# Kernel tuning notes

Measured on AMD Instinct MI355X. Metric: run time of the kernel, lower is better.

## Reference

```python
import jax, jax.numpy as jnp
import numpy as np

EPS = 1e-5
GROUPS = 32
K = 7  # correlation kernel size (min(7, 14))


def group_norm(x, w, b):
    B, C, H, W = x.shape
    xg = x.reshape(B, GROUPS, C // GROUPS, H, W)
    m = xg.mean(axis=(2, 3, 4), keepdims=True)
    v = xg.var(axis=(2, 3, 4), keepdims=True)
    xg = (xg - m) * jax.lax.rsqrt(v + EPS)
    return xg.reshape(B, C, H, W) * w[None, :, None, None] + b[None, :, None, None]


def conv1x1(x, w):  # w: [O, C]
    return jnp.einsum('bchw,oc->bohw', x, w)


def setup_inputs() -> dict:
    key = jax.random.key(0)
    ks = jax.random.split(key, 16)
    C, CC = 256, 64
    d = {}
    d['template_feat'] = jax.random.normal(ks[0], (32, C, 14, 14), jnp.float32)
    d['search_feat'] = jax.random.normal(ks[1], (32, C, 64, 64), jnp.float32)
    s1 = 1.0 / np.sqrt(C)
    d['w_t'] = jax.random.normal(ks[2], (CC, C), jnp.float32) * s1
    d['gn_t_w'] = jnp.ones((CC,), jnp.float32)
    d['gn_t_b'] = jnp.zeros((CC,), jnp.float32)
    d['w_s'] = jax.random.normal(ks[3], (CC, C), jnp.float32) * s1
    d['gn_s_w'] = jnp.ones((CC,), jnp.float32)
    d['gn_s_b'] = jnp.zeros((CC,), jnp.float32)
    d['w_p1'] = jax.random.normal(ks[4], (CC, CC, 3, 3), jnp.float32) * (1.0 / np.sqrt(CC * 9))
    d['gn_p_w'] = jnp.ones((CC,), jnp.float32)
    d['gn_p_b'] = jnp.zeros((CC,), jnp.float32)
    d['w_p2'] = jax.random.normal(ks[5], (1, CC), jnp.float32) * (1.0 / np.sqrt(CC))
    d['b_p2'] = jnp.zeros((1,), jnp.float32)
    return d


def reference(template_feat, search_feat, w_t, gn_t_w, gn_t_b, w_s, gn_s_w, gn_s_b,
              w_p1, gn_p_w, gn_p_b, w_p2, b_p2):
    B, _, Hs, Ws = search_feat.shape
    CC = w_t.shape[0]

    t = jax.nn.relu(group_norm(conv1x1(template_feat, w_t), gn_t_w, gn_t_b))   # [B,CC,14,14]
    s = jax.nn.relu(group_norm(conv1x1(search_feat, w_s), gn_s_w, gn_s_b))     # [B,CC,Hs,Ws]

    # global correlation: adaptive pool template to (1,1) == mean
    t_global = t.mean(axis=(2, 3), keepdims=True)
    global_corr = s * t_global

    # local depthwise correlation: adaptive pool 14x14 -> 7x7 (exact 2x2 mean)
    Ht = t.shape[2]
    r = Ht // K
    t_kernel = t.reshape(B, CC, K, r, K, r).mean(axis=(3, 5))                  # [B,CC,7,7]

    # batched per-sample depthwise conv: fold batch into groups
    x = s.reshape(1, B * CC, Hs, Ws)
    kern = t_kernel.reshape(B * CC, 1, K, K)
    local = jax.lax.conv_general_dilated(
        x, kern, window_strides=(1, 1), padding=[(K // 2, K // 2)] * 2,
        dimension_numbers=('NCHW', 'OIHW', 'NCHW'),
        feature_group_count=B * CC)
    local_corr = local.reshape(B, CC, Hs, Ws)

    corr = global_corr + local_corr

    # post_corr: 3x3 conv -> GN -> ReLU -> 1x1 conv (+bias)
    y = jax.lax.conv_general_dilated(
        corr, w_p1, window_strides=(1, 1), padding='SAME',
        dimension_numbers=('NCHW', 'OIHW', 'NCHW'))
    y = jax.nn.relu(group_norm(y, gn_p_w, gn_p_b))
    out = conv1x1(y, w_p2) + b_p2[None, :, None, None]                          # [B,1,Hs,Ws]
    return out
```

## Files before the change

### kernel.cpp

```cpp
#include <hip/hip_runtime.h>

#define EPS 1e-5f


typedef __attribute__((ext_vector_type(8))) short short8;
typedef __attribute__((ext_vector_type(4))) float floatx4;

__device__ __forceinline__ unsigned short f2bf(float x) {
    union { float f; unsigned u; } v; v.f = x;
    unsigned r = v.u + 0x7FFFu + ((v.u >> 16) & 1u);
    return (unsigned short)(r >> 16);
}
__device__ __forceinline__ float bf2f(unsigned short h) {
    union { unsigned u; float f; } v; v.u = ((unsigned)h) << 16;
    return v.f;
}

__global__ __launch_bounds__(256) void k1_template(
    const float* __restrict__ tmpl, const float* __restrict__ w_t,
    const float* __restrict__ gnw, const float* __restrict__ gnb,
    float* __restrict__ t_global, float* __restrict__ t_kernel)
{
    int b = blockIdx.x >> 1, h = blockIdx.x & 1;
    int tid = threadIdx.x;
    __shared__ float T[32][197];
    __shared__ float sums[32], sumsq[32], A[32], Bb[32];
    int p = tid;
    if (p < 196) {
        float acc[32];
        #pragma unroll
        for (int o = 0; o < 32; ++o) acc[o] = 0.f;
        const float* xb = tmpl + b * 256 * 196 + p;
        const float* wb = w_t + (h * 32) * 256;
        for (int c = 0; c < 256; ++c) {
            float xv = xb[c * 196];
            #pragma unroll
            for (int o = 0; o < 32; ++o) acc[o] += xv * wb[o * 256 + c];
        }
        #pragma unroll
        for (int o = 0; o < 32; ++o) T[o][p] = acc[o];
    }
    __syncthreads();
    if (tid < 32) {
        float s = 0.f, s2 = 0.f;
        for (int q = 0; q < 196; ++q) { float v = T[tid][q]; s += v; s2 += v * v; }
        sums[tid] = s; sumsq[tid] = s2;
    }
    __syncthreads();
    if (tid < 16) {
        float S  = sums[2 * tid] + sums[2 * tid + 1];
        float S2 = sumsq[2 * tid] + sumsq[2 * tid + 1];
        float mean = S * (1.f / 392.f);
        float var  = S2 * (1.f / 392.f) - mean * mean;
        float inv  = rsqrtf(var + EPS);
        for (int e = 0; e < 2; ++e) {
            int c = 2 * tid + e, gc = h * 32 + c;
            float a = gnw[gc] * inv;
            A[c] = a; Bb[c] = gnb[gc] - mean * a;
        }
    }
    __syncthreads();
    if (p < 196) {
        #pragma unroll
        for (int o = 0; o < 32; ++o) {
            float v = A[o] * T[o][p] + Bb[o];
            T[o][p] = v > 0.f ? v : 0.f;
        }
    }
    __syncthreads();
    if (tid < 32) {
        int c = tid, gc = h * 32 + c;
        float s = 0.f;
        for (int q = 0; q < 196; ++q) s += T[c][q];
        t_global[b * 64 + gc] = s * (1.f / 196.f);
        for (int t = 0; t < 49; ++t) {
            int ky = t / 7, kx = t - 7 * ky;
            float v = T[c][(2 * ky) * 14 + 2 * kx]     + T[c][(2 * ky) * 14 + 2 * kx + 1]
                    + T[c][(2 * ky + 1) * 14 + 2 * kx] + T[c][(2 * ky + 1) * 14 + 2 * kx + 1];
            t_kernel[(b * 64 + gc) * 49 + t] = v * 0.25f;
        }
    }
}

__global__ __launch_bounds__(256) void k2_gemm_s(
    const float* __restrict__ x, const float* __restrict__ w,
    float* __restrict__ sraw)
{
    int b = blockIdx.y;
    int p0 = blockIdx.x << 8;
    int tid = threadIdx.x;
    int tx = tid & 31, ty = tid >> 5;
    __shared__ float Xs[16][256];
    __shared__ float Ws[16][68];
    float acc[8][8];
    #pragma unroll
    for (int j = 0; j < 8; ++j)
        #pragma unroll
        for (int k = 0; k < 8; ++k) acc[j][k] = 0.f;
    const float* xb = x + ((long)b << 20) + p0;
    for (int c0 = 0; c0 < 256; c0 += 16) {
        __syncthreads();
        #pragma unroll
        for (int l = 0; l < 16; ++l)
            Xs[l][tid] = xb[(c0 + l) * 4096 + tid];
        #pragma unroll
        for (int l = 0; l < 4; ++l) {
            int flat = tid + (l << 8);
            int o = flat >> 4, cc = flat & 15;
            Ws[cc][o] = w[o * 256 + c0 + cc];
        }
        __syncthreads();
        #pragma unroll
        for (int cc = 0; cc < 16; ++cc) {
            float xv[8], wv[8];
            #pragma unroll
            for (int k = 0; k < 8; ++k) xv[k] = Xs[cc][tx + (k << 5)];
            #pragma unroll
            for (int j = 0; j < 8; ++j) wv[j] = Ws[cc][(ty << 3) + j];
            #pragma unroll
            for (int j = 0; j < 8; ++j)
                #pragma unroll
                for (int k = 0; k < 8; ++k) acc[j][k] += wv[j] * xv[k];
        }
    }
    float* ob = sraw + ((long)b << 18) + p0;
    #pragma unroll
    for (int j = 0; j < 8; ++j) {
        int o = (ty << 3) + j;
        #pragma unroll
        for (int k = 0; k < 8; ++k)
            ob[(o << 12) + tx + (k << 5)] = acc[j][k];
    }
}

__global__ __launch_bounds__(256) void k_stats(
    const float* __restrict__ src, const float* __restrict__ gnw, const float* __restrict__ gnb,
    float* __restrict__ A, float* __restrict__ Bc)
{
    int g = blockIdx.x, b = blockIdx.y;
    int tid = threadIdx.x;
    const float* base = src + (((long)b * 64 + 2 * g) << 12);
    float s = 0.f, s2 = 0.f;
    for (int l = 0; l < 32; ++l) {
        float v = base[tid + (l << 8)];
        s += v; s2 += v * v;
    }
    #pragma unroll
    for (int off = 32; off > 0; off >>= 1) {
        s  += __shfl_down(s, off, 64);
        s2 += __shfl_down(s2, off, 64);
    }
    __shared__ float rs[4], rs2[4];
    int wid = tid >> 6, lane = tid & 63;
    if (lane == 0) { rs[wid] = s; rs2[wid] = s2; }
    __syncthreads();
    if (tid == 0) {
        float S = rs[0] + rs[1] + rs[2] + rs[3];
        float S2 = rs2[0] + rs2[1] + rs2[2] + rs2[3];
        float mean = S * (1.f / 8192.f);
        float var  = S2 * (1.f / 8192.f) - mean * mean;
        float inv  = rsqrtf(var + EPS);
        for (int e = 0; e < 2; ++e) {
            int c = 2 * g + e;
            float a = gnw[c] * inv;
            A[b * 64 + c] = a;
            Bc[b * 64 + c] = gnb[c] - mean * a;
        }
    }
}

__global__ __launch_bounds__(256) void k4_corr(
    const float* __restrict__ sraw, const float* __restrict__ A, const float* __restrict__ Bc,
    const float* __restrict__ t_global, const float* __restrict__ t_kernel,
    float* __restrict__ corr)
{
    int bc = blockIdx.x;
    int tid = threadIdx.x;
    __shared__ float tile[70 * 70];
    __shared__ float ker[49];
    float a = A[bc], bb = Bc[bc], tg = t_global[bc];
    for (int i = tid; i < 4900; i += 256) tile[i] = 0.f;
    if (tid < 49) ker[tid] = t_kernel[bc * 49 + tid];
    __syncthreads();
    const float* sb = sraw + ((long)bc << 12);
    for (int i = tid; i < 4096; i += 256) {
        int y = i >> 6, xx = i & 63;
        float v = a * sb[i] + bb;
        tile[(y + 3) * 70 + xx + 3] = v > 0.f ? v : 0.f;
    }
    __syncthreads();
    int x = tid & 63, ys = (tid >> 6) << 4;
    float acc[16];
    #pragma unroll
    for (int j = 0; j < 16; ++j) acc[j] = 0.f;
    #pragma unroll
    for (int kx = 0; kx < 7; ++kx) {
        float col[22];
        #pragma unroll
        for (int j = 0; j < 22; ++j) col[j] = tile[(ys + j) * 70 + x + kx];
        #pragma unroll
        for (int ky = 0; ky < 7; ++ky) {
            float kv = ker[ky * 7 + kx];
            #pragma unroll
            for (int j = 0; j < 16; ++j) acc[j] += kv * col[j + ky];
        }
    }
    float* ob = corr + ((long)bc << 12);
    #pragma unroll
    for (int j = 0; j < 16; ++j) {
        float sval = tile[(ys + j + 3) * 70 + x + 3];
        ob[((ys + j) << 6) + x] = acc[j] + sval * tg;
    }
}

__global__ __launch_bounds__(256) void k_t(
    const float* __restrict__ corr, unsigned short* __restrict__ corrT)
{
    int py = blockIdx.x, b = blockIdx.y;
    int tid = threadIdx.x;
    __shared__ float T[64][65];
    {
        int c0 = tid >> 6, px = tid & 63;
        const float* src = corr + (((long)b * 64) << 12) + (py << 6) + px;
        #pragma unroll
        for (int i = 0; i < 16; ++i) {
            int c = c0 + (i << 2);
            T[c][px] = src[(long)c << 12];
        }
    }
    __syncthreads();
    int ob = tid & 7, pxw = tid >> 3;
    unsigned short* dst = corrT + ((((b << 12)) + (py << 6)) << 6);
    #pragma unroll
    for (int i = 0; i < 2; ++i) {
        int p = pxw + (i << 5);
        unsigned w0 = (unsigned)f2bf(T[8 * ob + 0][p]) | ((unsigned)f2bf(T[8 * ob + 1][p]) << 16);
        unsigned w1 = (unsigned)f2bf(T[8 * ob + 2][p]) | ((unsigned)f2bf(T[8 * ob + 3][p]) << 16);
        unsigned w2 = (unsigned)f2bf(T[8 * ob + 4][p]) | ((unsigned)f2bf(T[8 * ob + 5][p]) << 16);
        unsigned w3 = (unsigned)f2bf(T[8 * ob + 6][p]) | ((unsigned)f2bf(T[8 * ob + 7][p]) << 16);
        uint4 val = {w0, w1, w2, w3};
        *(uint4*)(dst + ((long)p << 6) + (ob << 3)) = val;
    }
}

__global__ __launch_bounds__(256) void k_w(
    const float* __restrict__ w1, unsigned short* __restrict__ wpk)
{
    int i = blockIdx.x * 256 + threadIdx.x;
    if (i >= 36864) return;
    int c = i >> 11;
    int rem = i & 2047;
    int oc = rem >> 5;
    int k = rem & 31;
    int tap = c >> 1;
    int ic = ((c & 1) << 5) + k;
    wpk[i] = f2bf(w1[oc * 576 + ic * 9 + tap]);
}

__global__ __launch_bounds__(256) void k5_mfma(
    const unsigned short* __restrict__ corrT, const unsigned short* __restrict__ wpk,
    unsigned short* __restrict__ y)
{
    int b = blockIdx.y, py0 = blockIdx.x << 2;
    int tid = threadIdx.x;
    int wave = tid >> 6, lane = tid & 63, q = lane >> 4, l15 = lane & 15;
    __shared__ short tile[25344];

    for (int u = tid; u < 3168; u += 256) {
        int icblk = u & 7, rc = u >> 3;
        int row = rc / 66, col = rc - 66 * row;
        int py = py0 - 1 + row, px = col - 1;
        short8 v = {0, 0, 0, 0, 0, 0, 0, 0};
        if (py >= 0 && py < 64 && px >= 0 && px < 64)
            v = *(const short8*)(corrT + (((b << 12) + (py << 6) + px) << 6) + (icblk << 3));
        int sw = icblk ^ (col & 7);
        *(short8*)&tile[(rc << 6) + (sw << 3)] = v;
    }
    __syncthreads();

    floatx4 acc[4][4];
    #pragma unroll
    for (int i = 0; i < 4; ++i)
        #pragma unroll
        for (int ot = 0; ot < 4; ++ot) acc[i][ot] = (floatx4){0.f, 0.f, 0.f, 0.f};

    int pt0 = wave << 2;
    int rowb[4], colb[4];
    #pragma unroll
    for (int i = 0; i < 4; ++i) {
        int p = ((pt0 + i) << 4) + l15;
        rowb[i] = p >> 6;
        colb[i] = p & 63;
    }
    #pragma unroll
    for (int c = 0; c < 18; ++c) {
        const int tap = c >> 1, ky = tap / 3, kx = tap % 3, h = c & 1;
        short8 bfr[4], afr[4];
        #pragma unroll
        for (int ot = 0; ot < 4; ++ot)
            bfr[ot] = *(const short8*)(wpk + ((c << 6) + (ot << 4) + l15) * 32 + (q << 3));
        #pragma unroll
        for (int i = 0; i < 4; ++i) {
            int row = rowb[i] + ky, col = colb[i] + kx;
            int sw = ((h << 2) + q) ^ (col & 7);
            afr[i] = *(const short8*)&tile[((row * 66 + col) << 6) + (sw << 3)];
        }
        #pragma unroll
        for (int i = 0; i < 4; ++i)
            #pragma unroll
            for (int ot = 0; ot < 4; ++ot)
                acc[i][ot] = __builtin_amdgcn_mfma_f32_16x16x32_bf16(afr[i], bfr[ot], acc[i][ot], 0, 0, 0);
    }
    #pragma unroll
    for (int i = 0; i < 4; ++i) {
        #pragma unroll
        for (int r = 0; r < 4; ++r) {
            int p = ((pt0 + i) << 4) + (q << 2) + r;
            int py = py0 + (p >> 6), pxc = p & 63;
            int base = ((b << 12) + (py << 6) + pxc) << 6;
            #pragma unroll
            for (int ot = 0; ot < 4; ++ot)
                y[base + (ot << 4) + l15] = f2bf(acc[i][ot][r]);
        }
    }
}

__global__ __launch_bounds__(256) void k_sy1(
    const unsigned short* __restrict__ y, float* __restrict__ P1, float* __restrict__ P2)
{
    int sl = blockIdx.x, b = blockIdx.y;
    int tid = threadIdx.x;
    int ocp = tid & 31, px0 = tid >> 5;
    const unsigned* yp = (const unsigned*)y;
    float se = 0, s2e = 0, so = 0, s2o = 0;
    for (int k = 0; k < 64; ++k) {
        int px = (sl << 9) + (k << 3) + px0;
        unsigned u = yp[(((b << 12) + px) << 5) + ocp];
        float f0 = bf2f((unsigned short)(u & 0xFFFF));
        float f1 = bf2f((unsigned short)(u >> 16));
        se += f0; s2e += f0 * f0; so += f1; s2o += f1 * f1;
    }
    se += __shfl_down(se, 32, 64);  s2e += __shfl_down(s2e, 32, 64);
    so += __shfl_down(so, 32, 64);  s2o += __shfl_down(s2o, 32, 64);
    __shared__ float R[4][32][4];
    int w = tid >> 6, l = tid & 63;
    if (l < 32) { R[w][l][0] = se; R[w][l][1] = s2e; R[w][l][2] = so; R[w][l][3] = s2o; }
    __syncthreads();
    if (tid < 32) {
        float a0 = 0, a1 = 0, a2 = 0, a3 = 0;
        for (int w2 = 0; w2 < 4; ++w2) {
            a0 += R[w2][tid][0]; a1 += R[w2][tid][1]; a2 += R[w2][tid][2]; a3 += R[w2][tid][3];
        }
        int idx = ((b << 3) + sl) << 6;
        P1[idx + 2 * tid]     = a0; P2[idx + 2 * tid]     = a1;
        P1[idx + 2 * tid + 1] = a2; P2[idx + 2 * tid + 1] = a3;
    }
}

__global__ __launch_bounds__(64) void k_sy2(
    const float* __restrict__ P1, const float* __restrict__ P2,
    const float* __restrict__ gnw, const float* __restrict__ gnb,
    float* __restrict__ A, float* __restrict__ Bc)
{
    int b = blockIdx.x, c = threadIdx.x;
    float s = 0, s2 = 0;
    for (int sl = 0; sl < 8; ++sl) {
        int idx = (((b << 3) + sl) << 6) + c;
        s += P1[idx]; s2 += P2[idx];
    }
    float sp = __shfl_xor(s, 1, 64), s2p = __shfl_xor(s2, 1, 64);
    float S = s + sp, S2 = s2 + s2p;
    float mean = S * (1.f / 8192.f);
    float var  = S2 * (1.f / 8192.f) - mean * mean;
    float inv  = rsqrtf(var + EPS);
    float a = gnw[c] * inv;
    A[b * 64 + c] = a;
    Bc[b * 64 + c] = gnb[c] - mean * a;
}

__global__ __launch_bounds__(256) void k6_nhwc(
    const unsigned short* __restrict__ y, const float* __restrict__ A, const float* __restrict__ Bc,
    const float* __restrict__ w2, const float* __restrict__ b2, float* __restrict__ out)
{
    int b = blockIdx.y;
    int px0 = blockIdx.x << 9;
    int tid = threadIdx.x, wave = tid >> 6, lane = tid & 63;
    int ocp = lane & 31, ph = lane >> 5;
    int c0 = 2 * ocp;
    float a0 = A[b * 64 + c0],     b0 = Bc[b * 64 + c0],     w20 = w2[c0];
    float a1 = A[b * 64 + c0 + 1], b1 = Bc[b * 64 + c0 + 1], w21 = w2[c0 + 1];
    float bias = b2[0];
    const unsigned* yp = (const unsigned*)y;
    for (int i = 0; i < 64; ++i) {
        int px = px0 + (i << 3) + (wave << 1) + ph;
        unsigned u = yp[(((b << 12) + px) << 5) + ocp];
        float f0 = bf2f((unsigned short)(u & 0xFFFF));
        float f1 = bf2f((unsigned short)(u >> 16));
        float v0 = a0 * f0 + b0; v0 = v0 > 0.f ? v0 : 0.f;
        float v1 = a1 * f1 + b1; v1 = v1 > 0.f ? v1 : 0.f;
        float val = w20 * v0 + w21 * v1;
        #pragma unroll
        for (int m = 16; m >= 1; m >>= 1) val += __shfl_xor(val, m, 64);
        if (ocp == 0) out[(b << 12) + px] = val + bias;
    }
}

extern "C" void kernel_launch(void* const* d_in, const int* in_sizes, int n_in,
                              void* d_out, int out_size, void* d_ws, size_t ws_size,
                              hipStream_t stream)
{
    const float* tmpl   = (const float*)d_in[0];
    const float* search = (const float*)d_in[1];
    const float* w_t    = (const float*)d_in[2];
    const float* gn_t_w = (const float*)d_in[3];
    const float* gn_t_b = (const float*)d_in[4];
    const float* w_s    = (const float*)d_in[5];
    const float* gn_s_w = (const float*)d_in[6];
    const float* gn_s_b = (const float*)d_in[7];
    const float* w_p1   = (const float*)d_in[8];
    const float* gn_p_w = (const float*)d_in[9];
    const float* gn_p_b = (const float*)d_in[10];
    const float* w_p2   = (const float*)d_in[11];
    const float* b_p2   = (const float*)d_in[12];
    float* out = (float*)d_out;
    float* ws  = (float*)d_ws;

    float* TG   = ws;
    float* TK   = ws + 2048;
    float* AS   = ws + 102400;
    float* BS   = ws + 104448;
    float* AY   = ws + 106496;
    float* BY   = ws + 108544;
    float* P1   = ws + 110592;
    float* P2   = ws + 126976;
    unsigned short* WPK = (unsigned short*)(ws + 143360);
    float* SRAW = ws + 163840;
    float* CORR = ws + 163840 + 8388608;
    unsigned short* YRAW  = (unsigned short*)SRAW;
    unsigned short* CORRT = (unsigned short*)(SRAW + 4194304);

    k1_template<<<64, 256, 0, stream>>>(tmpl, w_t, gn_t_w, gn_t_b, TG, TK);
    k_w<<<144, 256, 0, stream>>>(w_p1, WPK);
    k2_gemm_s<<<dim3(16, 32), 256, 0, stream>>>(search, w_s, SRAW);
    k_stats<<<dim3(32, 32), 256, 0, stream>>>(SRAW, gn_s_w, gn_s_b, AS, BS);
    k4_corr<<<2048, 256, 0, stream>>>(SRAW, AS, BS, TG, TK, CORR);
    k_t<<<dim3(64, 32), 256, 0, stream>>>(CORR, CORRT);
    k5_mfma<<<dim3(16, 32), 256, 0, stream>>>(CORRT, WPK, YRAW);
    k_sy1<<<dim3(8, 32), 256, 0, stream>>>(YRAW, P1, P2);
    k_sy2<<<32, 64, 0, stream>>>(P1, P2, gn_p_w, gn_p_b, AY, BY);
    k6_nhwc<<<dim3(8, 32), 256, 0, stream>>>(YRAW, AY, BY, w_p2, b_p2, out);
}
```

Measured before the change: 440.4 us.

## Use bf16 MFMA for search 1x1 conv and split template kernel finer

Replaces the fp32 register-tiled GEMM for the search-feature 1x1 conv with a bf16 MFMA kernel. Activations are converted to bf16 into a swizzled LDS tile, and a small pre-kernel converts the weights to bf16 in workspace. The template kernel is also restructured to handle 16 output channels per block (128 blocks) and to stage inputs through LDS with float4 loads. This targets the compute cost of the large 1x1 conv, at the price of bf16 rounding of inputs and weights.

Result: faster. 361.4 us (-17.9%).

```diff
diff --git a/kernel.cpp b/kernel.cpp
--- a/kernel.cpp
+++ b/kernel.cpp
@@ -21,40 +21,58 @@
     const float* __restrict__ gnw, const float* __restrict__ gnb,
     float* __restrict__ t_global, float* __restrict__ t_kernel)
 {
-    int b = blockIdx.x >> 1, h = blockIdx.x & 1;
-    int tid = threadIdx.x;
-    __shared__ float T[32][197];
-    __shared__ float sums[32], sumsq[32], A[32], Bb[32];
+    int b = blockIdx.x >> 2, h = blockIdx.x & 3;
+    int tid = threadIdx.x;
+    __shared__ float Xs[32][200];
+    __shared__ float T[16][200];
+    __shared__ float sums[16], sumsq[16], A[16], Bb[16];
+    float acc[16];
+    #pragma unroll
+    for (int o = 0; o < 16; ++o) acc[o] = 0.f;
+    const float* wb = w_t + (h * 16) * 256;
+    const float* tb = tmpl + b * 50176;
     int p = tid;
+    for (int chunk = 0; chunk < 8; ++chunk) {
+        __syncthreads();
+        #pragma unroll
+        for (int j = 0; j < 7; ++j) {
+            int f4 = tid + (j << 8);
+            if (f4 < 1568) {
+                int ic = f4 / 49, px4 = (f4 - ic * 49) << 2;
+                float4 v = *(const float4*)(tb + (chunk * 32 + ic) * 196 + px4);
+                *(float4*)&Xs[ic][px4] = v;
+            }
+        }
+        __syncthreads();
+        if (p < 196) {
+            for (int cc = 0; cc < 32; ++cc) {
+                float xv = Xs[cc][p];
+                #pragma unroll
+                for (int o = 0; o < 16; ++o)
+                    acc[o] += xv * wb[o * 256 + chunk * 32 + cc];
+            }
+        }
+    }
+    __syncthreads();
     if (p < 196) {
-        float acc[32];
-        #pragma unroll
-        for (int o = 0; o < 32; ++o) acc[o] = 0.f;
-        const float* xb = tmpl + b * 256 * 196 + p;
-        const float* wb = w_t + (h * 32) * 256;
-        for (int c = 0; c < 256; ++c) {
-            float xv = xb[c * 196];
-            #pragma unroll
-            for (int o = 0; o < 32; ++o) acc[o] += xv * wb[o * 256 + c];
-        }
-        #pragma unroll
-        for (int o = 0; o < 32; ++o) T[o][p] = acc[o];
-    }
-    __syncthreads();
-    if (tid < 32) {
+        #pragma unroll
+        for (int o = 0; o < 16; ++o) T[o][p] = acc[o];
+    }
+    __syncthreads();
+    if (tid < 16) {
         float s = 0.f, s2 = 0.f;
         for (int q = 0; q < 196; ++q) { float v = T[tid][q]; s += v; s2 += v * v; }
         sums[tid] = s; sumsq[tid] = s2;
     }
     __syncthreads();
-    if (tid < 16) {
+    if (tid < 8) {
         float S  = sums[2 * tid] + sums[2 * tid + 1];
         float S2 = sumsq[2 * tid] + sumsq[2 * tid + 1];
         float mean = S * (1.f / 392.f);
         float var  = S2 * (1.f / 392.f) - mean * mean;
         float inv  = rsqrtf(var + EPS);
         for (int e = 0; e < 2; ++e) {
-            int c = 2 * tid + e, gc = h * 32 + c;
+            int c = 2 * tid + e, gc = h * 16 + c;
             float a = gnw[gc] * inv;
             A[c] = a; Bb[c] = gnb[gc] - mean * a;
         }
@@ -62,14 +80,14 @@
     __syncthreads();
     if (p < 196) {
         #pragma unroll
-        for (int o = 0; o < 32; ++o) {
+        for (int o = 0; o < 16; ++o) {
             float v = A[o] * T[o][p] + Bb[o];
             T[o][p] = v > 0.f ? v : 0.f;
         }
     }
     __syncthreads();
-    if (tid < 32) {
-        int c = tid, gc = h * 32 + c;
+    if (tid < 16) {
+        int c = tid, gc = h * 16 + c;
         float s = 0.f;
         for (int q = 0; q < 196; ++q) s += T[c][q];
         t_global[b * 64 + gc] = s * (1.f / 196.f);
@@ -82,54 +100,79 @@
     }
 }
 
-__global__ __launch_bounds__(256) void k2_gemm_s(
-    const float* __restrict__ x, const float* __restrict__ w,
+__global__ __launch_bounds__(256) void k_w2(
+    const float* __restrict__ w, unsigned short* __restrict__ wsb)
+{
+    int i = blockIdx.x * 256 + threadIdx.x;
+    if (i < 16384) wsb[i] = f2bf(w[i]);
+}
+
+__global__ __launch_bounds__(256) void k2_mfma(
+    const float* __restrict__ x, const unsigned short* __restrict__ wsb,
     float* __restrict__ sraw)
 {
-    int b = blockIdx.y;
-    int p0 = blockIdx.x << 8;
-    int tid = threadIdx.x;
-    int tx = tid & 31, ty = tid >> 5;
-    __shared__ float Xs[16][256];
-    __shared__ float Ws[16][68];
-    float acc[8][8];
-    #pragma unroll
-    for (int j = 0; j < 8; ++j)
-        #pragma unroll
-        for (int k = 0; k < 8; ++k) acc[j][k] = 0.f;
-    const float* xb = x + ((long)b << 20) + p0;
-    for (int c0 = 0; c0 < 256; c0 += 16) {
+    int b = blockIdx.y, p0 = blockIdx.x << 8;
+    int tid = threadIdx.x;
+    int wave = tid >> 6, lane = tid & 63, q = lane >> 4, l15 = lane & 15;
+    __shared__ short tile[256 * 64];
+
+    floatx4 acc[4][4];
+    #pragma unroll
+    for (int i = 0; i < 4; ++i)
+        #pragma unroll
+        for (int mt = 0; mt < 4; ++mt) acc[i][mt] = (floatx4){0.f, 0.f, 0.f, 0.f};
+
+    const float* xb = x + ((long)b << 20) + p0 + tid;
+    for (int chunk = 0; chunk < 4; ++chunk) {
         __syncthreads();
         #pragma unroll
-        for (int l = 0; l < 16; ++l)
-            Xs[l][tid] = xb[(c0 + l) * 4096 + tid];
-        #pragma unroll
-        for (int l = 0; l < 4; ++l) {
-            int flat = tid + (l << 8);
-            int o = flat >> 4, cc = flat & 15;
-            Ws[cc][o] = w[o * 256 + c0 + cc];
+        for (int half = 0; half < 2; ++half) {
+            float v[32];
+            #pragma unroll
+            for (int i = 0; i < 32; ++i)
+                v[i] = xb[(long)((chunk << 6) + (half << 5) + i) << 12];
+            #pragma unroll
+            for (int blk = 0; blk < 4; ++blk) {
+                int icblk = (half << 2) + blk;
+                short8 s;
+                #pragma unroll
+                for (int e = 0; e < 8; ++e) s[e] = (short)f2bf(v[(blk << 3) + e]);
+                int sw = icblk ^ (tid & 7);
+                *(short8*)&tile[(tid << 6) + (sw << 3)] = s;
+            }
         }
         __syncthreads();
         #pragma unroll
-        for (int cc = 0; cc < 16; ++cc) {
-            float xv[8], wv[8];
-            #pragma unroll
-            for (int k = 0; k < 8; ++k) xv[k] = Xs[cc][tx + (k << 5)];
-            #pragma unroll
-            for (int j = 0; j < 8; ++j) wv[j] = Ws[cc][(ty << 3) + j];
-            #pragma unroll
-            for (int j = 0; j < 8; ++j)
+        for (int kq = 0; kq < 2; ++kq) {
+            short8 afr[4], bfr[4];
+            int kbase = (chunk << 6) + (kq << 5) + (q << 3);
+            #pragma unroll
+            for (int mt = 0; mt < 4; ++mt)
+                afr[mt] = *(const short8*)(wsb + ((mt << 4) + l15) * 256 + kbase);
+            #pragma unroll
+            for (int i = 0; i < 4; ++i) {
+                int px = (((wave << 2) + i) << 4) + l15;
+                int sw = ((kq << 2) + q) ^ (px & 7);
+                bfr[i] = *(const short8*)&tile[(px << 6) + (sw << 3)];
+            }
+            #pragma unroll
+            for (int i = 0; i < 4; ++i)
                 #pragma unroll
-                for (int k = 0; k < 8; ++k) acc[j][k] += wv[j] * xv[k];
+                for (int mt = 0; mt < 4; ++mt)
+                    acc[i][mt] = __builtin_amdgcn_mfma_f32_16x16x32_bf16(afr[mt], bfr[i], acc[i][mt], 0, 0, 0);
         }
     }
     float* ob = sraw + ((long)b << 18) + p0;
     #pragma unroll
-    for (int j = 0; j < 8; ++j) {
-        int o = (ty << 3) + j;
-        #pragma unroll
-        for (int k = 0; k < 8; ++k)
-            ob[(o << 12) + tx + (k << 5)] = acc[j][k];
+    for (int i = 0; i < 4; ++i) {
+        int pxb = ((wave << 2) + i) << 4;
+        #pragma unroll
+        for (int mt = 0; mt < 4; ++mt)
+            #pragma unroll
+            for (int r = 0; r < 4; ++r) {
+                int oc = (mt << 4) + (q << 2) + r;
+                ob[(oc << 12) + pxb + l15] = acc[i][mt][r];
+            }
     }
 }
 
@@ -438,10 +481,12 @@
     float* CORR = ws + 163840 + 8388608;
     unsigned short* YRAW  = (unsigned short*)SRAW;
     unsigned short* CORRT = (unsigned short*)(SRAW + 4194304);
-
-    k1_template<<<64, 256, 0, stream>>>(tmpl, w_t, gn_t_w, gn_t_b, TG, TK);
+    unsigned short* WSB   = (unsigned short*)CORR;
+
+    k_w2<<<64, 256, 0, stream>>>(w_s, WSB);
+    k1_template<<<128, 256, 0, stream>>>(tmpl, w_t, gn_t_w, gn_t_b, TG, TK);
     k_w<<<144, 256, 0, stream>>>(w_p1, WPK);
-    k2_gemm_s<<<dim3(16, 32), 256, 0, stream>>>(search, w_s, SRAW);
+    k2_mfma<<<dim3(16, 32), 256, 0, stream>>>(search, WSB, SRAW);
     k_stats<<<dim3(32, 32), 256, 0, stream>>>(SRAW, gn_s_w, gn_s_b, AS, BS);
     k4_corr<<<2048, 256, 0, stream>>>(SRAW, AS, BS, TG, TK, CORR);
     k_t<<<dim3(64, 32), 256, 0, stream>>>(CORR, CORRT);
```
